# Optimization experiments

Measured on AMD Instinct MI355X. Metric: run time of the kernel, lower is better.

Reference implementation:

```python
import jax, jax.numpy as jnp
import numpy as np


def graph_conv(x, W, b, src, dst, n_nodes):
    """DGL GraphConv, norm='both', activation=relu.
    Pre-scale by out-degree^-1/2 of src, project (in>out so project first),
    sum-aggregate over edges, post-scale by in-degree^-1/2 of dst."""
    ones = jnp.ones(src.shape[0], dtype=x.dtype)
    deg_out = jax.ops.segment_sum(ones, src, num_segments=n_nodes)
    deg_in = jax.ops.segment_sum(ones, dst, num_segments=n_nodes)
    norm_src = jnp.clip(deg_out, 1.0, None) ** -0.5  # [N]
    norm_dst = jnp.clip(deg_in, 1.0, None) ** -0.5   # [N]
    h = x * norm_src[:, None]
    h = h @ W  # project first since in_feats > out_feats
    # message passing: gather src features, scatter-add into dst
    agg = jax.ops.segment_sum(h[src], dst, num_segments=n_nodes)  # [N, out]
    agg = agg * norm_dst[:, None]
    return jax.nn.relu(agg + b)


def setup_inputs() -> dict:
    key = jax.random.key(0)
    ks = jax.random.split(key, 6)
    N, E, D_IN, D_HID = 50000, 800000, 1024, 256
    x = jax.random.normal(ks[0], (N, D_IN), dtype=jnp.float32)
    src = jax.random.randint(ks[1], (E,), 0, N)
    dst = jax.random.randint(ks[2], (E,), 0, N)
    # Glorot-style init for weights
    W1 = jax.random.normal(ks[3], (D_IN, D_HID), dtype=jnp.float32) * (1.0 / np.sqrt(D_IN))
    b1 = jnp.zeros((D_HID,), dtype=jnp.float32)
    W2 = jax.random.normal(ks[4], (D_HID, 1), dtype=jnp.float32) * (1.0 / np.sqrt(D_HID))
    b2 = jnp.zeros((1,), dtype=jnp.float32)
    return {"x": x, "src": src, "dst": dst, "W1": W1, "b1": b1, "W2": W2, "b2": b2, "n_nodes": N}


def reference(x, src, dst, W1, b1, W2, b2, n_nodes):
    h = graph_conv(x, W1, b1, src, dst, n_nodes)   # [N, 256]
    out = graph_conv(h, W2, b2, src, dst, n_nodes)  # [N, 1]
    return out
```

## Files before the change

### kernel.cpp

```cpp
#include <hip/hip_runtime.h>
#include <hip/hip_bf16.h>

typedef __attribute__((ext_vector_type(8))) short bf16x8;
typedef __attribute__((ext_vector_type(4))) float f32x4;

static __device__ __forceinline__ short f2bf(float f) {
    unsigned u = __float_as_uint(f);
    unsigned r = (u + 0x7FFFu + ((u >> 16) & 1u)) >> 16;
    return (short)(unsigned short)r;
}
static __device__ __forceinline__ float bf2f(short s) {
    return __uint_as_float(((unsigned)(unsigned short)s) << 16);
}

static __device__ __forceinline__ void gload16(const void* g, void* l) {
    __builtin_amdgcn_global_load_lds((const __attribute__((address_space(1))) unsigned int*)g,
                                     (__attribute__((address_space(3))) unsigned int*)l, 16, 0, 0);
}

static __device__ __forceinline__ bf16x8 cvt8(const f32x4 lo, const f32x4 hi) {
    __hip_bfloat162 p0 = __float22bfloat162_rn(make_float2(lo[0], lo[1]));
    __hip_bfloat162 p1 = __float22bfloat162_rn(make_float2(lo[2], lo[3]));
    __hip_bfloat162 p2 = __float22bfloat162_rn(make_float2(hi[0], hi[1]));
    __hip_bfloat162 p3 = __float22bfloat162_rn(make_float2(hi[2], hi[3]));
    short2 s0 = *(short2*)&p0, s1 = *(short2*)&p1, s2 = *(short2*)&p2, s3 = *(short2*)&p3;
    bf16x8 r = {s0.x, s0.y, s1.x, s1.y, s2.x, s2.y, s3.x, s3.y};
    return r;
}

__global__ void deg_kernel(const int* __restrict__ src, const int* __restrict__ dst,
                           int* __restrict__ deg_out, int* __restrict__ deg_in, int E) {
    int e = blockIdx.x * blockDim.x + threadIdx.x;
    if (e < E) {
        atomicAdd(&deg_out[src[e]], 1);
        atomicAdd(&deg_in[dst[e]], 1);
    }
}

__global__ void norm_kernel(const int* __restrict__ deg_out, const int* __restrict__ deg_in,
                            float* __restrict__ ns, float* __restrict__ nd, int N) {
    int i = blockIdx.x * blockDim.x + threadIdx.x;
    if (i < N) {
        ns[i] = rsqrtf((float)max(deg_out[i], 1));
        nd[i] = rsqrtf((float)max(deg_in[i], 1));
    }
}

__global__ void scan_part1(const int* __restrict__ deg, int* __restrict__ bsum, int N) {
    __shared__ int red[256];
    int i = blockIdx.x * 256 + threadIdx.x;
    red[threadIdx.x] = (i < N) ? deg[i] : 0;
    __syncthreads();
    for (int off = 128; off > 0; off >>= 1) {
        if (threadIdx.x < off) red[threadIdx.x] += red[threadIdx.x + off];
        __syncthreads();
    }
    if (threadIdx.x == 0) bsum[blockIdx.x] = red[0];
}

__global__ void scan_part2(const int* __restrict__ bsum, int* __restrict__ bsum_ex, int NB,
                           int* __restrict__ offsets, int N, int E) {
    __shared__ int s[256];
    int t = threadIdx.x;
    int v = (t < NB) ? bsum[t] : 0;
    s[t] = v;
    __syncthreads();
    for (int off = 1; off < 256; off <<= 1) {
        int u = (t >= off) ? s[t - off] : 0;
        __syncthreads();
        s[t] += u;
        __syncthreads();
    }
    bsum_ex[t] = s[t] - v;
    if (t == 0) offsets[N] = E;
}

__global__ void scan_part3(const int* __restrict__ deg, const int* __restrict__ bsum_ex,
                           int* __restrict__ offsets, int N) {
    __shared__ int s[256];
    int t = threadIdx.x, i = blockIdx.x * 256 + t;
    int v = (i < N) ? deg[i] : 0;
    s[t] = v;
    __syncthreads();
    for (int off = 1; off < 256; off <<= 1) {
        int u = (t >= off) ? s[t - off] : 0;
        __syncthreads();
        s[t] += u;
        __syncthreads();
    }
    if (i < N) offsets[i] = bsum_ex[blockIdx.x] + s[t] - v;
}

__global__ void scatter_kernel(const int* __restrict__ src, const int* __restrict__ dst,
                               const int* __restrict__ offsets, int* __restrict__ cursor,
                               int* __restrict__ bucket, int E) {
    int e = blockIdx.x * blockDim.x + threadIdx.x;
    if (e < E) {
        int d = dst[e];
        int p = atomicAdd(&cursor[d], 1);
        bucket[offsets[d] + p] = src[e];
    }
}

__global__ __launch_bounds__(1024) void transpose_w1(const float* __restrict__ W1,
                                                     short* __restrict__ Wt) {
    __shared__ short tile[32][33];
    int k0 = blockIdx.x * 32, n0 = blockIdx.y * 32;
    int tx = threadIdx.x & 31, ty = threadIdx.x >> 5;
    tile[ty][tx] = f2bf(W1[(size_t)(k0 + ty) * 256 + (n0 + tx)]);
    __syncthreads();
    Wt[(size_t)(n0 + ty) * 1024 + (k0 + tx)] = tile[tx][ty];
}

#define BM 128
#define BN 128
#define BK 32
#define CSTR 136

union SMem {
    struct {
        float A[BM * BK];
        short B[BN * BK];
    } s;
    short C[BM * CSTR];
};

__global__ __launch_bounds__(256, 3) void gemm1_kernel(const float* __restrict__ x,
                                                       const short* __restrict__ Wt,
                                                       const float* __restrict__ norm_src,
                                                       short* __restrict__ hb, int M) {
    __shared__ __align__(16) SMem sm;
    __shared__ float ns_lds[BM];
    const int tid  = threadIdx.x;
    const int lane = tid & 63;
    const int wave = tid >> 6;
    const int quad = lane >> 4;
    const int mrow = lane & 15;
    const int wm = (wave >> 1) * 64;
    const int wn = (wave & 1) * 64;
    const int bm = blockIdx.x * BM;
    const int bn = blockIdx.y * BN;

    if (tid < BM) ns_lds[tid] = norm_src[min(bm + tid, M - 1)];

    f32x4 acc[4][4] = {};

    const int aL_r = lane >> 3;
    const int aL_c = (lane & 7) ^ (aL_r & 7);
    const int bL_r = lane >> 2;
    const int bL_c = (lane & 3) ^ ((lane >> 3) & 3);

    for (int k0 = 0; k0 < 1024; k0 += BK) {
#pragma unroll
        for (int i = 0; i < 4; i++) {
            int rowbase = wave * 32 + i * 8;
            int r = rowbase + aL_r;
            if (bm + r < M)
                gload16(x + (size_t)(bm + r) * 1024 + k0 + aL_c * 4, &sm.s.A[rowbase * 32]);
        }
#pragma unroll
        for (int i = 0; i < 2; i++) {
            int nbase = wave * 32 + i * 16;
            int n = nbase + bL_r;
            gload16(Wt + (size_t)(bn + n) * 1024 + k0 + bL_c * 8, &sm.s.B[nbase * 32]);
        }
        __syncthreads();

        bf16x8 af[4], bfr[4];
#pragma unroll
        for (int mi = 0; mi < 4; mi++) {
            int row = wm + mi * 16 + mrow;
            f32x4 lo = *(const f32x4*)&sm.s.A[row * 32 + (((quad * 2 + 0) ^ (mrow & 7)) * 4)];
            f32x4 hi = *(const f32x4*)&sm.s.A[row * 32 + (((quad * 2 + 1) ^ (mrow & 7)) * 4)];
            af[mi] = cvt8(lo, hi);
        }
#pragma unroll
        for (int ni = 0; ni < 4; ni++) {
            int n = wn + ni * 16 + mrow;
            bfr[ni] = *(const bf16x8*)&sm.s.B[n * 32 + ((quad ^ ((mrow >> 1) & 3)) * 8)];
        }
#pragma unroll
        for (int mi = 0; mi < 4; mi++)
#pragma unroll
            for (int ni = 0; ni < 4; ni++)
                acc[mi][ni] = __builtin_amdgcn_mfma_f32_16x16x32_bf16(af[mi], bfr[ni], acc[mi][ni], 0, 0, 0);
        __syncthreads();
    }

#pragma unroll
    for (int mi = 0; mi < 4; mi++) {
#pragma unroll
        for (int reg = 0; reg < 4; reg++) {
            int row = wm + mi * 16 + quad * 4 + reg;
            float nsv = ns_lds[row];
#pragma unroll
            for (int ni = 0; ni < 4; ni++) {
                int col = wn + ni * 16 + mrow;
                sm.C[row * CSTR + col] = f2bf(acc[mi][ni][reg] * nsv);
            }
        }
    }
    __syncthreads();
#pragma unroll
    for (int j = 0; j < 8; j++) {
        int row = wave * 4 + (lane >> 4) + j * 16;
        int chunk = lane & 15;
        if (bm + row < M) {
            int4 v = *(const int4*)&sm.C[row * CSTR + chunk * 8];
            *(int4*)(hb + (size_t)(bm + row) * 256 + bn + chunk * 8) = v;
        }
    }
}

__global__ __launch_bounds__(256) void agg1_kernel(const short* __restrict__ hb,
                                                   const int* __restrict__ bucket,
                                                   const int* __restrict__ offsets,
                                                   const float* __restrict__ norm_dst,
                                                   const float* __restrict__ norm_src,
                                                   const float* __restrict__ b1,
                                                   const float* __restrict__ W2,
                                                   float* __restrict__ z, int N) {
    int wave = threadIdx.x >> 6;
    int lane = threadIdx.x & 63;
    int node = blockIdx.x * 4 + wave;
    if (node >= N) return;
    int beg = offsets[node], end = offsets[node + 1];
    float a0 = 0.f, a1 = 0.f, a2 = 0.f, a3 = 0.f;
    int e = beg;
    for (; e + 3 < end; e += 4) {
        int s0 = bucket[e], s1 = bucket[e + 1], s2 = bucket[e + 2], s3 = bucket[e + 3];
        short4 v0 = *(const short4*)(hb + (size_t)s0 * 256 + lane * 4);
        short4 v1 = *(const short4*)(hb + (size_t)s1 * 256 + lane * 4);
        short4 v2 = *(const short4*)(hb + (size_t)s2 * 256 + lane * 4);
        short4 v3 = *(const short4*)(hb + (size_t)s3 * 256 + lane * 4);
        a0 += bf2f(v0.x) + bf2f(v1.x) + bf2f(v2.x) + bf2f(v3.x);
        a1 += bf2f(v0.y) + bf2f(v1.y) + bf2f(v2.y) + bf2f(v3.y);
        a2 += bf2f(v0.z) + bf2f(v1.z) + bf2f(v2.z) + bf2f(v3.z);
        a3 += bf2f(v0.w) + bf2f(v1.w) + bf2f(v2.w) + bf2f(v3.w);
    }
    for (; e < end; e++) {
        short4 v0 = *(const short4*)(hb + (size_t)bucket[e] * 256 + lane * 4);
        a0 += bf2f(v0.x); a1 += bf2f(v0.y); a2 += bf2f(v0.z); a3 += bf2f(v0.w);
    }
    float nd = norm_dst[node];
    float4 bb = *(const float4*)(b1 + lane * 4);
    float o0 = fmaxf(a0 * nd + bb.x, 0.f);
    float o1 = fmaxf(a1 * nd + bb.y, 0.f);
    float o2 = fmaxf(a2 * nd + bb.z, 0.f);
    float o3 = fmaxf(a3 * nd + bb.w, 0.f);
    float4 w = *(const float4*)(W2 + lane * 4);
    float p = o0 * w.x + o1 * w.y + o2 * w.z + o3 * w.w;
#pragma unroll
    for (int off = 32; off > 0; off >>= 1) p += __shfl_xor(p, off, 64);
    if (lane == 0) z[node] = p * norm_src[node];
}

__global__ void agg2_kernel(const float* __restrict__ z, const int* __restrict__ bucket,
                            const int* __restrict__ offsets, const float* __restrict__ norm_dst,
                            const float* __restrict__ b2, float* __restrict__ out, int N) {
    int i = blockIdx.x * blockDim.x + threadIdx.x;
    if (i >= N) return;
    int beg = offsets[i], end = offsets[i + 1];
    float s = 0.f;
    for (int e = beg; e < end; e++) s += z[bucket[e]];
    out[i] = fmaxf(s * norm_dst[i] + b2[0], 0.f);
}

extern "C" void kernel_launch(void* const* d_in, const int* in_sizes, int n_in,
                              void* d_out, int out_size, void* d_ws, size_t ws_size,
                              hipStream_t stream) {
    const int D_HID = in_sizes[4];
    const int D_IN  = in_sizes[3] / D_HID;
    const int N     = in_sizes[0] / D_IN;
    const int E     = in_sizes[1];

    const float* x   = (const float*)d_in[0];
    const int*   src = (const int*)d_in[1];
    const int*   dst = (const int*)d_in[2];
    const float* W1  = (const float*)d_in[3];
    const float* b1  = (const float*)d_in[4];
    const float* W2  = (const float*)d_in[5];
    const float* b2  = (const float*)d_in[6];
    float* out = (float*)d_out;

    char* p = (char*)d_ws;
    auto alloc = [&](size_t bytes) {
        void* r = (void*)p;
        p += (bytes + 255) & ~(size_t)255;
        return r;
    };
    int*   deg_out  = (int*)alloc((size_t)N * 4);
    int*   deg_in   = (int*)alloc((size_t)N * 4);
    int*   cursor   = (int*)alloc((size_t)N * 4);
    float* norm_src = (float*)alloc((size_t)N * 4);
    float* norm_dst = (float*)alloc((size_t)N * 4);
    int*   offsets  = (int*)alloc((size_t)(N + 1) * 4);
    int*   bucket   = (int*)alloc((size_t)E * 4);
    short* Wt       = (short*)alloc((size_t)D_IN * D_HID * 2);
    short* hb       = (short*)alloc((size_t)N * D_HID * 2);
    float* z        = (float*)alloc((size_t)N * 4);
    int*   bsum     = (int*)alloc(256 * 4);
    int*   bsum_ex  = (int*)alloc(256 * 4);

    const int NB = (N + 255) / 256;

    hipMemsetAsync(deg_out, 0, (size_t)N * 4, stream);
    hipMemsetAsync(deg_in,  0, (size_t)N * 4, stream);
    hipMemsetAsync(cursor,  0, (size_t)N * 4, stream);

    deg_kernel<<<(E + 255) / 256, 256, 0, stream>>>(src, dst, deg_out, deg_in, E);
    norm_kernel<<<(N + 255) / 256, 256, 0, stream>>>(deg_out, deg_in, norm_src, norm_dst, N);
    scan_part1<<<NB, 256, 0, stream>>>(deg_in, bsum, N);
    scan_part2<<<1, 256, 0, stream>>>(bsum, bsum_ex, NB, offsets, N, E);
    scan_part3<<<NB, 256, 0, stream>>>(deg_in, bsum_ex, offsets, N);
    scatter_kernel<<<(E + 255) / 256, 256, 0, stream>>>(src, dst, offsets, cursor, bucket, E);
    transpose_w1<<<dim3(D_IN / 32, D_HID / 32), 1024, 0, stream>>>(W1, Wt);
    gemm1_kernel<<<dim3((N + BM - 1) / BM, D_HID / BN), 256, 0, stream>>>(x, Wt, norm_src, hb, N);
    agg1_kernel<<<(N + 3) / 4, 256, 0, stream>>>(hb, bucket, offsets, norm_dst, norm_src, b1, W2, z, N);
    agg2_kernel<<<(N + 255) / 256, 256, 0, stream>>>(z, bucket, offsets, norm_dst, b2, out, N);
}
```

Before: 517.7 us.

## Use full-width GEMM tiles, widen gather loads, fuse norm into scan, merge memsets

The GEMM tile changes from 128x128 to 64x256, so each block covers the full hidden width and the fp32 x matrix is streamed once instead of twice. The aggregation kernel now loads 16-byte bf16x8 vectors, with each half-wave handling a different edge, and combines the halves with a cross-lane shuffle. The norm computation moves into the final scan kernel, and three memsets become one contiguous memset. The cost is fewer GEMM blocks and larger per-wave accumulators, which may reduce occupancy.

```diff
diff --git a/kernel.cpp b/kernel.cpp
--- a/kernel.cpp
+++ b/kernel.cpp
@@ -37,15 +37,6 @@
     }
 }
 
-__global__ void norm_kernel(const int* __restrict__ deg_out, const int* __restrict__ deg_in,
-                            float* __restrict__ ns, float* __restrict__ nd, int N) {
-    int i = blockIdx.x * blockDim.x + threadIdx.x;
-    if (i < N) {
-        ns[i] = rsqrtf((float)max(deg_out[i], 1));
-        nd[i] = rsqrtf((float)max(deg_in[i], 1));
-    }
-}
-
 __global__ void scan_part1(const int* __restrict__ deg, int* __restrict__ bsum, int N) {
     __shared__ int red[256];
     int i = blockIdx.x * 256 + threadIdx.x;
@@ -75,11 +66,12 @@
     if (t == 0) offsets[N] = E;
 }
 
-__global__ void scan_part3(const int* __restrict__ deg, const int* __restrict__ bsum_ex,
-                           int* __restrict__ offsets, int N) {
+__global__ void scan_part3(const int* __restrict__ deg_in, const int* __restrict__ deg_out,
+                           const int* __restrict__ bsum_ex, int* __restrict__ offsets,
+                           float* __restrict__ ns, float* __restrict__ nd, int N) {
     __shared__ int s[256];
     int t = threadIdx.x, i = blockIdx.x * 256 + t;
-    int v = (i < N) ? deg[i] : 0;
+    int v = (i < N) ? deg_in[i] : 0;
     s[t] = v;
     __syncthreads();
     for (int off = 1; off < 256; off <<= 1) {
@@ -88,7 +80,11 @@
         s[t] += u;
         __syncthreads();
     }
-    if (i < N) offsets[i] = bsum_ex[blockIdx.x] + s[t] - v;
+    if (i < N) {
+        offsets[i] = bsum_ex[blockIdx.x] + s[t] - v;
+        ns[i] = rsqrtf((float)max(deg_out[i], 1));
+        nd[i] = rsqrtf((float)max(v, 1));
+    }
 }
 
 __global__ void scatter_kernel(const int* __restrict__ src, const int* __restrict__ dst,
@@ -112,10 +108,10 @@
     Wt[(size_t)(n0 + ty) * 1024 + (k0 + tx)] = tile[tx][ty];
 }
 
-#define BM 128
-#define BN 128
+#define BM 64
+#define BN 256
 #define BK 32
-#define CSTR 136
+#define CSTR 264
 
 union SMem {
     struct {
@@ -136,14 +132,13 @@
     const int wave = tid >> 6;
     const int quad = lane >> 4;
     const int mrow = lane & 15;
-    const int wm = (wave >> 1) * 64;
-    const int wn = (wave & 1) * 64;
+    const int wm = (wave >> 1) * 32;
+    const int wn = (wave & 1) * 128;
     const int bm = blockIdx.x * BM;
-    const int bn = blockIdx.y * BN;
 
     if (tid < BM) ns_lds[tid] = norm_src[min(bm + tid, M - 1)];
 
-    f32x4 acc[4][4] = {};
+    f32x4 acc[2][8] = {};
 
     const int aL_r = lane >> 3;
     const int aL_c = (lane & 7) ^ (aL_r & 7);
@@ -152,49 +147,49 @@
 
     for (int k0 = 0; k0 < 1024; k0 += BK) {
 #pragma unroll
-        for (int i = 0; i < 4; i++) {
-            int rowbase = wave * 32 + i * 8;
+        for (int i = 0; i < 2; i++) {
+            int rowbase = wave * 16 + i * 8;
             int r = rowbase + aL_r;
             if (bm + r < M)
                 gload16(x + (size_t)(bm + r) * 1024 + k0 + aL_c * 4, &sm.s.A[rowbase * 32]);
         }
 #pragma unroll
-        for (int i = 0; i < 2; i++) {
-            int nbase = wave * 32 + i * 16;
+        for (int i = 0; i < 4; i++) {
+            int nbase = wave * 64 + i * 16;
             int n = nbase + bL_r;
-            gload16(Wt + (size_t)(bn + n) * 1024 + k0 + bL_c * 8, &sm.s.B[nbase * 32]);
-        }
-        __syncthreads();
-
-        bf16x8 af[4], bfr[4];
-#pragma unroll
-        for (int mi = 0; mi < 4; mi++) {
+            gload16(Wt + (size_t)n * 1024 + k0 + bL_c * 8, &sm.s.B[nbase * 32]);
+        }
+        __syncthreads();
+
+        bf16x8 af[2], bfr[8];
+#pragma unroll
+        for (int mi = 0; mi < 2; mi++) {
             int row = wm + mi * 16 + mrow;
             f32x4 lo = *(const f32x4*)&sm.s.A[row * 32 + (((quad * 2 + 0) ^ (mrow & 7)) * 4)];
             f32x4 hi = *(const f32x4*)&sm.s.A[row * 32 + (((quad * 2 + 1) ^ (mrow & 7)) * 4)];
             af[mi] = cvt8(lo, hi);
         }
 #pragma unroll
-        for (int ni = 0; ni < 4; ni++) {
+        for (int ni = 0; ni < 8; ni++) {
             int n = wn + ni * 16 + mrow;
             bfr[ni] = *(const bf16x8*)&sm.s.B[n * 32 + ((quad ^ ((mrow >> 1) & 3)) * 8)];
         }
 #pragma unroll
-        for (int mi = 0; mi < 4; mi++)
-#pragma unroll
-            for (int ni = 0; ni < 4; ni++)
+        for (int mi = 0; mi < 2; mi++)
+#pragma unroll
+            for (int ni = 0; ni < 8; ni++)
                 acc[mi][ni] = __builtin_amdgcn_mfma_f32_16x16x32_bf16(af[mi], bfr[ni], acc[mi][ni], 0, 0, 0);
         __syncthreads();
     }
 
 #pragma unroll
-    for (int mi = 0; mi < 4; mi++) {
+    for (int mi = 0; mi < 2; mi++) {
 #pragma unroll
         for (int reg = 0; reg < 4; reg++) {
             int row = wm + mi * 16 + quad * 4 + reg;
             float nsv = ns_lds[row];
 #pragma unroll
-            for (int ni = 0; ni < 4; ni++) {
+            for (int ni = 0; ni < 8; ni++) {
                 int col = wn + ni * 16 + mrow;
                 sm.C[row * CSTR + col] = f2bf(acc[mi][ni][reg] * nsv);
             }
@@ -203,11 +198,11 @@
     __syncthreads();
 #pragma unroll
     for (int j = 0; j < 8; j++) {
-        int row = wave * 4 + (lane >> 4) + j * 16;
-        int chunk = lane & 15;
+        int row = wave * 2 + (lane >> 5) + j * 8;
+        int chunk = lane & 31;
         if (bm + row < M) {
             int4 v = *(const int4*)&sm.C[row * CSTR + chunk * 8];
-            *(int4*)(hb + (size_t)(bm + row) * 256 + bn + chunk * 8) = v;
+            *(int4*)(hb + (size_t)(bm + row) * 256 + chunk * 8) = v;
         }
     }
 }
@@ -222,36 +217,57 @@
                                                    float* __restrict__ z, int N) {
     int wave = threadIdx.x >> 6;
     int lane = threadIdx.x & 63;
+    int half = lane >> 5;
+    int col8 = lane & 31;
     int node = blockIdx.x * 4 + wave;
     if (node >= N) return;
     int beg = offsets[node], end = offsets[node + 1];
-    float a0 = 0.f, a1 = 0.f, a2 = 0.f, a3 = 0.f;
+    float a[8] = {0.f, 0.f, 0.f, 0.f, 0.f, 0.f, 0.f, 0.f};
     int e = beg;
-    for (; e + 3 < end; e += 4) {
-        int s0 = bucket[e], s1 = bucket[e + 1], s2 = bucket[e + 2], s3 = bucket[e + 3];
-        short4 v0 = *(const short4*)(hb + (size_t)s0 * 256 + lane * 4);
-        short4 v1 = *(const short4*)(hb + (size_t)s1 * 256 + lane * 4);
-        short4 v2 = *(const short4*)(hb + (size_t)s2 * 256 + lane * 4);
-        short4 v3 = *(const short4*)(hb + (size_t)s3 * 256 + lane * 4);
-        a0 += bf2f(v0.x) + bf2f(v1.x) + bf2f(v2.x) + bf2f(v3.x);
-        a1 += bf2f(v0.y) + bf2f(v1.y) + bf2f(v2.y) + bf2f(v3.y);
-        a2 += bf2f(v0.z) + bf2f(v1.z) + bf2f(v2.z) + bf2f(v3.z);
-        a3 += bf2f(v0.w) + bf2f(v1.w) + bf2f(v2.w) + bf2f(v3.w);
-    }
-    for (; e < end; e++) {
-        short4 v0 = *(const short4*)(hb + (size_t)bucket[e] * 256 + lane * 4);
-        a0 += bf2f(v0.x); a1 += bf2f(v0.y); a2 += bf2f(v0.z); a3 += bf2f(v0.w);
-    }
+    for (; e + 8 <= end; e += 8) {
+        int s0 = bucket[e + 0 + half];
+        int s1 = bucket[e + 2 + half];
+        int s2 = bucket[e + 4 + half];
+        int s3 = bucket[e + 6 + half];
+        bf16x8 v0 = *(const bf16x8*)(hb + (size_t)s0 * 256 + col8 * 8);
+        bf16x8 v1 = *(const bf16x8*)(hb + (size_t)s1 * 256 + col8 * 8);
+        bf16x8 v2 = *(const bf16x8*)(hb + (size_t)s2 * 256 + col8 * 8);
+        bf16x8 v3 = *(const bf16x8*)(hb + (size_t)s3 * 256 + col8 * 8);
+#pragma unroll
+        for (int j = 0; j < 8; j++)
+            a[j] += bf2f(v0[j]) + bf2f(v1[j]) + bf2f(v2[j]) + bf2f(v3[j]);
+    }
+    for (; e + 2 <= end; e += 2) {
+        int s0 = bucket[e + half];
+        bf16x8 v0 = *(const bf16x8*)(hb + (size_t)s0 * 256 + col8 * 8);
+#pragma unroll
+        for (int j = 0; j < 8; j++) a[j] += bf2f(v0[j]);
+    }
+    if (e < end && half == 0) {
+        int s0 = bucket[e];
+        bf16x8 v0 = *(const bf16x8*)(hb + (size_t)s0 * 256 + col8 * 8);
+#pragma unroll
+        for (int j = 0; j < 8; j++) a[j] += bf2f(v0[j]);
+    }
+#pragma unroll
+    for (int j = 0; j < 8; j++) a[j] += __shfl_xor(a[j], 32, 64);
+
     float nd = norm_dst[node];
-    float4 bb = *(const float4*)(b1 + lane * 4);
-    float o0 = fmaxf(a0 * nd + bb.x, 0.f);
-    float o1 = fmaxf(a1 * nd + bb.y, 0.f);
-    float o2 = fmaxf(a2 * nd + bb.z, 0.f);
-    float o3 = fmaxf(a3 * nd + bb.w, 0.f);
-    float4 w = *(const float4*)(W2 + lane * 4);
-    float p = o0 * w.x + o1 * w.y + o2 * w.z + o3 * w.w;
-#pragma unroll
-    for (int off = 32; off > 0; off >>= 1) p += __shfl_xor(p, off, 64);
+    float4 b_lo = *(const float4*)(b1 + col8 * 8);
+    float4 b_hi = *(const float4*)(b1 + col8 * 8 + 4);
+    float4 w_lo = *(const float4*)(W2 + col8 * 8);
+    float4 w_hi = *(const float4*)(W2 + col8 * 8 + 4);
+    float p = 0.f;
+    p += fmaxf(a[0] * nd + b_lo.x, 0.f) * w_lo.x;
+    p += fmaxf(a[1] * nd + b_lo.y, 0.f) * w_lo.y;
+    p += fmaxf(a[2] * nd + b_lo.z, 0.f) * w_lo.z;
+    p += fmaxf(a[3] * nd + b_lo.w, 0.f) * w_lo.w;
+    p += fmaxf(a[4] * nd + b_hi.x, 0.f) * w_hi.x;
+    p += fmaxf(a[5] * nd + b_hi.y, 0.f) * w_hi.y;
+    p += fmaxf(a[6] * nd + b_hi.z, 0.f) * w_hi.z;
+    p += fmaxf(a[7] * nd + b_hi.w, 0.f) * w_hi.w;
+#pragma unroll
+    for (int off = 16; off > 0; off >>= 1) p += __shfl_xor(p, off, 64);
     if (lane == 0) z[node] = p * norm_src[node];
 }
 
@@ -304,18 +320,16 @@
 
     const int NB = (N + 255) / 256;
 
-    hipMemsetAsync(deg_out, 0, (size_t)N * 4, stream);
-    hipMemsetAsync(deg_in,  0, (size_t)N * 4, stream);
-    hipMemsetAsync(cursor,  0, (size_t)N * 4, stream);
+    size_t degpad = ((size_t)N * 4 + 255) & ~(size_t)255;
+    hipMemsetAsync(deg_out, 0, degpad * 2 + (size_t)N * 4, stream);
 
     deg_kernel<<<(E + 255) / 256, 256, 0, stream>>>(src, dst, deg_out, deg_in, E);
-    norm_kernel<<<(N + 255) / 256, 256, 0, stream>>>(deg_out, deg_in, norm_src, norm_dst, N);
     scan_part1<<<NB, 256, 0, stream>>>(deg_in, bsum, N);
     scan_part2<<<1, 256, 0, stream>>>(bsum, bsum_ex, NB, offsets, N, E);
-    scan_part3<<<NB, 256, 0, stream>>>(deg_in, bsum_ex, offsets, N);
+    scan_part3<<<NB, 256, 0, stream>>>(deg_in, deg_out, bsum_ex, offsets, norm_src, norm_dst, N);
     scatter_kernel<<<(E + 255) / 256, 256, 0, stream>>>(src, dst, offsets, cursor, bucket, E);
     transpose_w1<<<dim3(D_IN / 32, D_HID / 32), 1024, 0, stream>>>(W1, Wt);
-    gemm1_kernel<<<dim3((N + BM - 1) / BM, D_HID / BN), 256, 0, stream>>>(x, Wt, norm_src, hb, N);
+    gemm1_kernel<<<dim3((N + BM - 1) / BM), 256, 0, stream>>>(x, Wt, norm_src, hb, N);
     agg1_kernel<<<(N + 3) / 4, 256, 0, stream>>>(hb, bucket, offsets, norm_dst, norm_src, b1, W2, z, N);
     agg2_kernel<<<(N + 255) / 256, 256, 0, stream>>>(z, bucket, offsets, norm_dst, b2, out, N);
 }
```

After: 513.7 us. No clear change (-0.8%).
